# Kernel tuning notes

Hardware: AMD Instinct MI355X
Metric: run time of the kernel (lower is better)

Reference implementation:

```python
import jax, jax.numpy as jnp
import numpy as np

N = 50000
E = 800000
NDIM_IN = 128
NDIM_OUT = 64
H = 3
EDIM = 8
CLASS_NUM = 10
NEG_SLOPE = 0.2  # DGL GATConv default negative_slope


def _gat_layer(src, dst, x, W, a_l, a_r, b):
    """One DGL-style GATConv layer. x: [N, Fin]; W: [Fin, H*D]; a_l/a_r: [H, D]; b: [H*D]."""
    n, hd = x.shape[0], W.shape[1]
    D = hd // H
    f = (x @ W).reshape(n, H, D)                         # projected feats [N,H,D]
    el = (f * a_l[None]).sum(-1)                          # [N,H]
    er = (f * a_r[None]).sum(-1)                          # [N,H]
    e = jax.nn.leaky_relu(el[src] + er[dst], NEG_SLOPE)   # [E,H] per-edge logits
    m = jax.ops.segment_max(e, dst, num_segments=n)       # softmax max per dst node
    ex = jnp.exp(e - m[dst])                              # [E,H]
    denom = jax.ops.segment_sum(ex, dst, num_segments=n)  # [N,H]
    alpha = ex / denom[dst]                               # edge softmax
    out = jax.ops.segment_sum(f[src] * alpha[:, :, None], dst, num_segments=n)  # [N,H,D]
    return out + b.reshape(1, H, D)


def setup_inputs() -> dict:
    key = jax.random.key(0)
    ks = jax.random.split(key, 16)
    src = jax.random.randint(ks[0], (E,), 0, N)
    dst = jax.random.randint(ks[1], (E,), 0, N)
    nfeats = jax.random.normal(ks[2], (N, NDIM_IN), dtype=jnp.float32)
    efeats = jax.random.normal(ks[3], (E, EDIM), dtype=jnp.float32)
    s1 = 1.0 / np.sqrt(NDIM_IN)
    s2 = 1.0 / np.sqrt(H * NDIM_OUT)
    sp = 1.0 / np.sqrt(2 * H * NDIM_OUT)
    W1 = jax.random.normal(ks[4], (NDIM_IN, H * NDIM_OUT), dtype=jnp.float32) * s1
    al1 = jax.random.normal(ks[5], (H, NDIM_OUT), dtype=jnp.float32) * s1
    ar1 = jax.random.normal(ks[6], (H, NDIM_OUT), dtype=jnp.float32) * s1
    b1 = jnp.zeros((H * NDIM_OUT,), dtype=jnp.float32)
    W2 = jax.random.normal(ks[7], (H * NDIM_OUT, H * NDIM_OUT), dtype=jnp.float32) * s2
    al2 = jax.random.normal(ks[8], (H, NDIM_OUT), dtype=jnp.float32) * s2
    ar2 = jax.random.normal(ks[9], (H, NDIM_OUT), dtype=jnp.float32) * s2
    b2 = jnp.zeros((H * NDIM_OUT,), dtype=jnp.float32)
    Wp = jax.random.normal(ks[10], (2 * H * NDIM_OUT, CLASS_NUM), dtype=jnp.float32) * sp
    bp = jnp.zeros((CLASS_NUM,), dtype=jnp.float32)
    return {"src": src, "dst": dst, "nfeats": nfeats, "efeats": efeats,
            "W1": W1, "al1": al1, "ar1": ar1, "b1": b1,
            "W2": W2, "al2": al2, "ar2": ar2, "b2": b2,
            "Wp": Wp, "bp": bp}


def reference(src, dst, nfeats, efeats, W1, al1, ar1, b1, W2, al2, ar2, b2, Wp, bp):
    # efeats is accepted but unused, matching the original forward signature.
    h = _gat_layer(src, dst, nfeats, W1, al1, ar1, b1)      # [N,H,D]
    h = jax.nn.relu(h.reshape(h.shape[0], -1))              # [N,H*D]
    h = _gat_layer(src, dst, h, W2, al2, ar2, b2)           # [N,H,D]
    h = jax.nn.relu(h.reshape(h.shape[0], -1))              # [N,H*D]
    # MLPPredictor: per-edge concat(src,dst) -> linear
    score = jnp.concatenate([h[src], h[dst]], axis=1) @ Wp + bp  # [E,class_num]
    return score
```

## Files before the change

kernel.cpp:

```cpp
#include <hip/hip_runtime.h>
#include <cstdint>

constexpr int KIN = 128;
constexpr int HD  = 192;
constexpr int NC  = 10;
#define NEG_SLOPE 0.2f

typedef __attribute__((ext_vector_type(8))) short bf16x8;
typedef __attribute__((ext_vector_type(4))) float f32x4;

__device__ __forceinline__ float b2f(unsigned short u) {
    union { unsigned int i; float f; } x; x.i = ((unsigned int)u) << 16; return x.f;
}
__device__ __forceinline__ float b2f_lo(unsigned int u) {
    union { unsigned int i; float f; } x; x.i = u << 16; return x.f;
}
__device__ __forceinline__ float b2f_hi(unsigned int u) {
    union { unsigned int i; float f; } x; x.i = u & 0xffff0000u; return x.f;
}
__device__ __forceinline__ unsigned short f2b(float f) {
    union { float f; unsigned int i; } x; x.f = f;
    unsigned int r = x.i + 0x7FFFu + ((x.i >> 16) & 1u);
    return (unsigned short)(r >> 16);
}
__device__ __forceinline__ float gload(const void* p, long i, int isbf) {
    return isbf ? b2f(((const unsigned short*)p)[i]) : ((const float*)p)[i];
}
__device__ __forceinline__ float lrelu(float v) { return v > 0.f ? v : NEG_SLOPE * v; }

__global__ void k_prep(const void* __restrict__ nfeats, const void* __restrict__ W1,
                       const void* __restrict__ W2, const void* __restrict__ Wp,
                       unsigned short* __restrict__ xb, int* __restrict__ deg,
                       unsigned short* __restrict__ Bp1, unsigned short* __restrict__ Bp2,
                       unsigned short* __restrict__ BpPQ, int N, long nx,
                       int bZ, int bC, int* __restrict__ flag) {
    __shared__ int shIsb;
    if (threadIdx.x == 0) {
        const unsigned short* u = (const unsigned short*)W1;
        float mx = 0.f;
        for (int i = 0; i < 64; ++i) {
            float v = fabsf(b2f(u[i]));
            if (!(v < 1e30f)) v = 1e30f;
            mx = fmaxf(mx, v);
        }
        shIsb = (mx < 1e4f) ? 1 : 0;
        if (blockIdx.x == 0) *flag = shIsb;
    }
    __syncthreads();
    int isb = shIsb;
    int b = blockIdx.x, tid = threadIdx.x;
    if (b < bZ) { int i = b * 256 + tid; if (i < N) deg[i] = 0; return; }
    b -= bZ;
    if (b < bC) {
        if (isb) return;
        long i = (long)b * 256 + tid;
        if (i < nx) xb[i] = f2b(gload(nfeats, i, isb));
        return;
    }
    b -= bC;
    int t = b * 256 + tid;
    const int s1 = 12 * 4 * 512, s2 = s1 + 12 * 6 * 512, s3 = s2 + 6 * 512, s4 = s3 + 6 * 512;
    const void* W; unsigned short* Bp; int K, Creal, KS; long rowOff; int tt;
    if (t < s1)      { W = W1; Bp = Bp1;            K = KIN; Creal = HD; KS = 4; rowOff = 0;  tt = t; }
    else if (t < s2) { W = W2; Bp = Bp2;            K = HD;  Creal = HD; KS = 6; rowOff = 0;  tt = t - s1; }
    else if (t < s3) { W = Wp; Bp = BpPQ;           K = HD;  Creal = NC; KS = 6; rowOff = 0;  tt = t - s2; }
    else if (t < s4) { W = Wp; Bp = BpPQ + 6 * 512; K = HD;  Creal = NC; KS = 6; rowOff = HD; tt = t - s3; }
    else return;
    int j = tt & 7, lane = (tt >> 3) & 63, ks = (tt >> 9) % KS, ct = tt / (KS * 512);
    int k = ks * 32 + ((lane >> 4) << 3) + j;
    int c = ct * 16 + (lane & 15);
    float v = 0.f;
    if (k < K && c < Creal) v = gload(W, (rowOff + k) * (long)Creal + c, isb);
    Bp[tt] = f2b(v);
}

template<int CT, int KS, int ELR>
__global__ void k_mm(const void* __restrict__ Ain, const unsigned short* __restrict__ xbA,
                     const unsigned short* __restrict__ Bp,
                     unsigned short* __restrict__ fb, const void* __restrict__ al,
                     const void* __restrict__ ar, float* __restrict__ el4,
                     float* __restrict__ er4, int M, int Cout, const int* __restrict__ flag) {
    int wid = threadIdx.x >> 6, lane = threadIdx.x & 63;
    int rt = blockIdx.x * 4 + wid;
    if (rt * 16 >= M) return;
    int isb = *flag;
    const unsigned short* A = isb ? (const unsigned short*)Ain : xbA;
    const int K = KS * 32;
    int mrow = rt * 16 + (lane & 15);
    int kq = (lane >> 4) << 3;
    f32x4 acc[CT];
#pragma unroll
    for (int ct = 0; ct < CT; ++ct) acc[ct] = (f32x4){0.f, 0.f, 0.f, 0.f};
    const unsigned short* arow = A + (long)mrow * K + kq;
    const bf16x8* bp = (const bf16x8*)Bp;
#pragma unroll
    for (int ks = 0; ks < KS; ++ks) {
        bf16x8 a = *(const bf16x8*)(arow + ks * 32);
#pragma unroll
        for (int ct = 0; ct < CT; ++ct) {
            bf16x8 b = bp[(ct * KS + ks) * 64 + lane];
            acc[ct] = __builtin_amdgcn_mfma_f32_16x16x32_bf16(a, b, acc[ct], 0, 0, 0);
        }
    }
    int quad = lane >> 4, c0 = lane & 15;
    int rbase = rt * 16 + quad * 4;
#pragma unroll
    for (int ct = 0; ct < CT; ++ct)
#pragma unroll
        for (int r = 0; r < 4; ++r)
            fb[(long)(rbase + r) * Cout + ct * 16 + c0] = f2b(acc[ct][r]);
    if (ELR) {
        float pl[3][4], pr[3][4];
#pragma unroll
        for (int h = 0; h < 3; ++h)
#pragma unroll
            for (int r = 0; r < 4; ++r) { pl[h][r] = 0.f; pr[h][r] = 0.f; }
#pragma unroll
        for (int ct = 0; ct < CT; ++ct) {
            int h = ct >> 2;
            float wl = gload(al, ct * 16 + c0, isb);
            float wr = gload(ar, ct * 16 + c0, isb);
#pragma unroll
            for (int r = 0; r < 4; ++r) {
                pl[h][r] += acc[ct][r] * wl;
                pr[h][r] += acc[ct][r] * wr;
            }
        }
#pragma unroll
        for (int d = 1; d < 16; d <<= 1)
#pragma unroll
            for (int h = 0; h < 3; ++h)
#pragma unroll
                for (int r = 0; r < 4; ++r) {
                    pl[h][r] += __shfl_xor(pl[h][r], d);
                    pr[h][r] += __shfl_xor(pr[h][r], d);
                }
        if (c0 == 0) {
#pragma unroll
            for (int r = 0; r < 4; ++r)
#pragma unroll
                for (int h = 0; h < 3; ++h) {
                    el4[(long)(rbase + r) * 4 + h] = pl[h][r];
                    er4[(long)(rbase + r) * 4 + h] = pr[h][r];
                }
        }
    }
}

__global__ void k_mmpq(const unsigned short* __restrict__ A, const unsigned short* __restrict__ Bp,
                       unsigned short* __restrict__ Pb, unsigned short* __restrict__ Qb, int M) {
    constexpr int CT = 2, KS = 6;
    int wid = threadIdx.x >> 6, lane = threadIdx.x & 63;
    int rt = blockIdx.x * 4 + wid;
    if (rt * 16 >= M) return;
    const int K = KS * 32;
    int mrow = rt * 16 + (lane & 15);
    int kq = (lane >> 4) << 3;
    f32x4 acc[CT];
#pragma unroll
    for (int ct = 0; ct < CT; ++ct) acc[ct] = (f32x4){0.f, 0.f, 0.f, 0.f};
    const unsigned short* arow = A + (long)mrow * K + kq;
    const bf16x8* bp = (const bf16x8*)Bp;
#pragma unroll
    for (int ks = 0; ks < KS; ++ks) {
        bf16x8 a = *(const bf16x8*)(arow + ks * 32);
#pragma unroll
        for (int ct = 0; ct < CT; ++ct) {
            bf16x8 b = bp[(ct * KS + ks) * 64 + lane];
            acc[ct] = __builtin_amdgcn_mfma_f32_16x16x32_bf16(a, b, acc[ct], 0, 0, 0);
        }
    }
    int quad = lane >> 4, c0 = lane & 15;
    int rbase = rt * 16 + quad * 4;
    if (c0 < NC) {
#pragma unroll
        for (int r = 0; r < 4; ++r) {
            Pb[(long)(rbase + r) * 16 + c0] = f2b(acc[0][r]);
            Qb[(long)(rbase + r) * 16 + c0] = f2b(acc[1][r]);
        }
    }
}

__global__ void k_hist(const int* __restrict__ dst, int E, int* __restrict__ deg) {
    int i = blockIdx.x * blockDim.x + threadIdx.x;
    if (i < E) atomicAdd(&deg[dst[i]], 1);
}

__global__ void k_scan1(const int* __restrict__ deg, int n, int* __restrict__ off,
                        int* __restrict__ bsum) {
    __shared__ int sh[1024];
    int tid = threadIdx.x, i = blockIdx.x * 1024 + tid;
    int v = (i < n) ? deg[i] : 0;
    sh[tid] = v;
    __syncthreads();
    for (int s = 1; s < 1024; s <<= 1) {
        int t = (tid >= s) ? sh[tid - s] : 0;
        __syncthreads();
        sh[tid] += t;
        __syncthreads();
    }
    if (i < n) off[i] = sh[tid] - v;
    if (tid == 1023) bsum[blockIdx.x] = sh[tid];
}

__global__ void k_scan2(int* __restrict__ bsum, int nb, int* __restrict__ off, int n) {
    int tid = threadIdx.x;
    int v = (tid < nb) ? bsum[tid] : 0;
    int incl = v;
    for (int s = 1; s < 64; s <<= 1) {
        int t = __shfl_up(incl, s);
        if (tid >= s) incl += t;
    }
    if (tid < nb) bsum[tid] = incl - v;
    if (tid == 63) off[n] = incl;
}

__global__ void k_scan3(int* __restrict__ off, const int* __restrict__ bsum, int n,
                        int* __restrict__ cur) {
    int i = blockIdx.x * 1024 + threadIdx.x;
    if (i < n) {
        int v = off[i] + bsum[blockIdx.x];
        off[i] = v;
        cur[i] = v;
    }
}

__global__ void k_fill(const int* __restrict__ src, const int* __restrict__ dst, int E,
                       int* __restrict__ cur, int* __restrict__ csr) {
    int i = blockIdx.x * blockDim.x + threadIdx.x;
    if (i < E) {
        int p = atomicAdd(&cur[dst[i]], 1);
        csr[p] = src[i];
    }
}

__global__ void k_agg(const unsigned int* __restrict__ fbu, const float4* __restrict__ el4,
                      const float* __restrict__ er4, const int* __restrict__ off,
                      const int* __restrict__ csr, const void* __restrict__ bias,
                      unsigned int* __restrict__ outu, int Nn, const int* __restrict__ flag) {
    __shared__ float4 shW[4][64];
    int lane = threadIdx.x & 63;
    int wv = threadIdx.x >> 6;
    int n = blockIdx.x * 4 + wv;
    if (n >= Nn) return;
    int isb = *flag;
    int s0 = off[n], s1 = off[n + 1];
    int deg = s1 - s0;
    float er0 = er4[n * 4 + 0], er1 = er4[n * 4 + 1], er2 = er4[n * 4 + 2];
    int hsel = lane >> 4;
    float a0 = 0.f, a1 = 0.f, a2 = 0.f, a3 = 0.f;

    if (deg <= 64) {
        bool on = lane < deg;
        int sIdx = on ? csr[s0 + lane] : 0;
        float4 el = el4[sIdx];
        float t0 = on ? lrelu(el.x + er0) : -1e30f;
        float t1 = on ? lrelu(el.y + er1) : -1e30f;
        float t2 = on ? lrelu(el.z + er2) : -1e30f;
        float m0 = t0, m1 = t1, m2 = t2;
        for (int d = 1; d < 64; d <<= 1) {
            m0 = fmaxf(m0, __shfl_xor(m0, d));
            m1 = fmaxf(m1, __shfl_xor(m1, d));
            m2 = fmaxf(m2, __shfl_xor(m2, d));
        }
        float w0 = on ? __expf(t0 - m0) : 0.f;
        float w1 = on ? __expf(t1 - m1) : 0.f;
        float w2 = on ? __expf(t2 - m2) : 0.f;
        float d0 = w0, d1 = w1, d2 = w2;
        for (int d = 1; d < 64; d <<= 1) {
            d0 += __shfl_xor(d0, d);
            d1 += __shfl_xor(d1, d);
            d2 += __shfl_xor(d2, d);
        }
        w0 *= 1.f / d0; w1 *= 1.f / d1; w2 *= 1.f / d2;
        shW[wv][lane] = make_float4(__int_as_float(sIdx), w0, w1, w2);
        if (lane < 48) {
            const float4* wr = shW[wv];
            long lb = 2 * lane;
            int j = 0;
            for (; j + 4 <= deg; j += 4) {
                float4 r0 = wr[j], r1 = wr[j + 1], r2 = wr[j + 2], r3 = wr[j + 3];
                uint2 u0 = *(const uint2*)(fbu + (long)__float_as_int(r0.x) * 96 + lb);
                uint2 u1 = *(const uint2*)(fbu + (long)__float_as_int(r1.x) * 96 + lb);
                uint2 u2 = *(const uint2*)(fbu + (long)__float_as_int(r2.x) * 96 + lb);
                uint2 u3 = *(const uint2*)(fbu + (long)__float_as_int(r3.x) * 96 + lb);
                float q0 = hsel == 0 ? r0.y : (hsel == 1 ? r0.z : r0.w);
                float q1 = hsel == 0 ? r1.y : (hsel == 1 ? r1.z : r1.w);
                float q2 = hsel == 0 ? r2.y : (hsel == 1 ? r2.z : r2.w);
                float q3 = hsel == 0 ? r3.y : (hsel == 1 ? r3.z : r3.w);
                a0 += q0 * b2f_lo(u0.x); a1 += q0 * b2f_hi(u0.x);
                a2 += q0 * b2f_lo(u0.y); a3 += q0 * b2f_hi(u0.y);
                a0 += q1 * b2f_lo(u1.x); a1 += q1 * b2f_hi(u1.x);
                a2 += q1 * b2f_lo(u1.y); a3 += q1 * b2f_hi(u1.y);
                a0 += q2 * b2f_lo(u2.x); a1 += q2 * b2f_hi(u2.x);
                a2 += q2 * b2f_lo(u2.y); a3 += q2 * b2f_hi(u2.y);
                a0 += q3 * b2f_lo(u3.x); a1 += q3 * b2f_hi(u3.x);
                a2 += q3 * b2f_lo(u3.y); a3 += q3 * b2f_hi(u3.y);
            }
            for (; j < deg; ++j) {
                float4 r0 = wr[j];
                uint2 u0 = *(const uint2*)(fbu + (long)__float_as_int(r0.x) * 96 + lb);
                float q0 = hsel == 0 ? r0.y : (hsel == 1 ? r0.z : r0.w);
                a0 += q0 * b2f_lo(u0.x); a1 += q0 * b2f_hi(u0.x);
                a2 += q0 * b2f_lo(u0.y); a3 += q0 * b2f_hi(u0.y);
            }
        }
    } else {
        float m0 = -1e30f, m1 = -1e30f, m2 = -1e30f;
        for (int e = s0 + lane; e < s1; e += 64) {
            float4 el = el4[csr[e]];
            m0 = fmaxf(m0, lrelu(el.x + er0));
            m1 = fmaxf(m1, lrelu(el.y + er1));
            m2 = fmaxf(m2, lrelu(el.z + er2));
        }
        for (int d = 1; d < 64; d <<= 1) {
            m0 = fmaxf(m0, __shfl_xor(m0, d));
            m1 = fmaxf(m1, __shfl_xor(m1, d));
            m2 = fmaxf(m2, __shfl_xor(m2, d));
        }
        float d0 = 0.f, d1 = 0.f, d2 = 0.f;
        for (int e = s0 + lane; e < s1; e += 64) {
            float4 el = el4[csr[e]];
            d0 += __expf(lrelu(el.x + er0) - m0);
            d1 += __expf(lrelu(el.y + er1) - m1);
            d2 += __expf(lrelu(el.z + er2) - m2);
        }
        for (int d = 1; d < 64; d <<= 1) {
            d0 += __shfl_xor(d0, d);
            d1 += __shfl_xor(d1, d);
            d2 += __shfl_xor(d2, d);
        }
        if (lane < 48) {
            float mh  = hsel == 0 ? m0 : (hsel == 1 ? m1 : m2);
            float dh  = hsel == 0 ? d0 : (hsel == 1 ? d1 : d2);
            float erh = hsel == 0 ? er0 : (hsel == 1 ? er1 : er2);
            float idh = 1.f / dh;
            long lb = 2 * lane;
            for (int e = s0; e < s1; ++e) {
                int s = csr[e];
                float4 el = el4[s];
                float eh = hsel == 0 ? el.x : (hsel == 1 ? el.y : el.z);
                float w = __expf(lrelu(eh + erh) - mh) * idh;
                uint2 u = *(const uint2*)(fbu + (long)s * 96 + lb);
                a0 += w * b2f_lo(u.x); a1 += w * b2f_hi(u.x);
                a2 += w * b2f_lo(u.y); a3 += w * b2f_hi(u.y);
            }
        }
    }
    if (lane < 48) {
        int c = 4 * lane;
        a0 = fmaxf(a0 + gload(bias, c,     isb), 0.f);
        a1 = fmaxf(a1 + gload(bias, c + 1, isb), 0.f);
        a2 = fmaxf(a2 + gload(bias, c + 2, isb), 0.f);
        a3 = fmaxf(a3 + gload(bias, c + 3, isb), 0.f);
        uint2 o;
        o.x = (unsigned)f2b(a0) | ((unsigned)f2b(a1) << 16);
        o.y = (unsigned)f2b(a2) | ((unsigned)f2b(a3) << 16);
        *(uint2*)(outu + (long)n * 96 + 2 * lane) = o;
    }
}

__global__ void k_score(const int* __restrict__ src, const int* __restrict__ dst,
                        const unsigned int* __restrict__ Pu, const unsigned int* __restrict__ Qu,
                        const void* __restrict__ bp, void* __restrict__ out,
                        int E, const int* __restrict__ flag) {
    __shared__ float sh[512 * NC];
    int tid = threadIdx.x;
    int e0 = blockIdx.x * 512;
    int isb = *flag;
    float bb[NC];
#pragma unroll
    for (int c = 0; c < NC; ++c) bb[c] = gload(bp, c, isb);

    float v[2][NC];
#pragma unroll
    for (int k = 0; k < 2; ++k) {
        int e = e0 + tid + k * 256;
        if (e < E) {
            const uint4* p4 = (const uint4*)(Pu + (long)src[e] * 8);
            const uint4* q4 = (const uint4*)(Qu + (long)dst[e] * 8);
            uint4 pa = p4[0]; unsigned int pb_ = Pu[(long)src[e] * 8 + 4];
            uint4 qa = q4[0]; unsigned int qb_ = Qu[(long)dst[e] * 8 + 4];
            v[k][0] = b2f_lo(pa.x) + b2f_lo(qa.x) + bb[0];
            v[k][1] = b2f_hi(pa.x) + b2f_hi(qa.x) + bb[1];
            v[k][2] = b2f_lo(pa.y) + b2f_lo(qa.y) + bb[2];
            v[k][3] = b2f_hi(pa.y) + b2f_hi(qa.y) + bb[3];
            v[k][4] = b2f_lo(pa.z) + b2f_lo(qa.z) + bb[4];
            v[k][5] = b2f_hi(pa.z) + b2f_hi(qa.z) + bb[5];
            v[k][6] = b2f_lo(pa.w) + b2f_lo(qa.w) + bb[6];
            v[k][7] = b2f_hi(pa.w) + b2f_hi(qa.w) + bb[7];
            v[k][8] = b2f_lo(pb_)  + b2f_lo(qb_)  + bb[8];
            v[k][9] = b2f_hi(pb_)  + b2f_hi(qb_)  + bb[9];
        }
    }
    int nE = min(512, E - e0);
    if (isb) {
        unsigned int* shu = (unsigned int*)sh;
#pragma unroll
        for (int k = 0; k < 2; ++k) {
            int le = tid + k * 256;
            if (e0 + le < E) {
#pragma unroll
                for (int c = 0; c < NC / 2; ++c)
                    shu[le * (NC / 2) + c] =
                        (unsigned)f2b(v[k][2 * c]) | ((unsigned)f2b(v[k][2 * c + 1]) << 16);
            }
        }
        __syncthreads();
        int nU = nE * (NC / 2);
        unsigned int* ob = (unsigned int*)((unsigned short*)out + (long)e0 * NC);
        int nU4 = nU >> 2;
        uint4* ob4 = (uint4*)ob;
        const uint4* sb4 = (const uint4*)shu;
        for (int u = tid; u < nU4; u += 256) ob4[u] = sb4[u];
        for (int w = (nU4 << 2) + tid; w < nU; w += 256) ob[w] = shu[w];
    } else {
#pragma unroll
        for (int k = 0; k < 2; ++k) {
            int le = tid + k * 256;
            if (e0 + le < E) {
#pragma unroll
                for (int c = 0; c < NC; ++c) sh[le * NC + c] = v[k][c];
            }
        }
        __syncthreads();
        int nU = nE * NC;
        float* ob = (float*)out + (long)e0 * NC;
        int nU4 = nU >> 2;
        float4* ob4 = (float4*)ob;
        const float4* sb4 = (const float4*)sh;
        for (int u = tid; u < nU4; u += 256) ob4[u] = sb4[u];
        for (int w = (nU4 << 2) + tid; w < nU; w += 256) ob[w] = sh[w];
    }
}

extern "C" void kernel_launch(void* const* d_in, const int* in_sizes, int n_in,
                              void* d_out, int out_size, void* d_ws, size_t ws_size,
                              hipStream_t stream) {
    const int* src = (const int*)d_in[0];
    const int* dst = (const int*)d_in[1];
    const void* nfeats = d_in[2];
    const void* W1  = d_in[4];
    const void* al1 = d_in[5];
    const void* ar1 = d_in[6];
    const void* b1  = d_in[7];
    const void* W2  = d_in[8];
    const void* al2 = d_in[9];
    const void* ar2 = d_in[10];
    const void* b2  = d_in[11];
    const void* Wp  = d_in[12];
    const void* bp  = d_in[13];

    const int E = in_sizes[0];
    const int N = in_sizes[2] / KIN;

    size_t o = 0;
    auto alloc = [&](size_t bytes) { size_t r = o; o = (o + bytes + 255) & ~(size_t)255; return r; };
    char* ws = (char*)d_ws;
    int*   flag = (int*)  (ws + alloc(4));
    int*   deg  = (int*)  (ws + alloc((size_t)N * 4));
    int*   off  = (int*)  (ws + alloc((size_t)(N + 1) * 4));
    int*   cur  = (int*)  (ws + alloc((size_t)N * 4));
    int*   bsum = (int*)  (ws + alloc(64 * 4));
    int*   csr  = (int*)  (ws + alloc((size_t)E * 4));
    unsigned short* xb  = (unsigned short*)(ws + alloc((size_t)N * KIN * 2));
    unsigned short* fb  = (unsigned short*)(ws + alloc((size_t)N * HD * 2));
    unsigned short* hb  = (unsigned short*)(ws + alloc((size_t)N * HD * 2));
    unsigned short* Bp1 = (unsigned short*)(ws + alloc((size_t)12 * 4 * 512 * 2));
    unsigned short* Bp2 = (unsigned short*)(ws + alloc((size_t)12 * 6 * 512 * 2));
    unsigned short* BpPQ= (unsigned short*)(ws + alloc((size_t)2 * 6 * 512 * 2));
    float* el4  = (float*)(ws + alloc((size_t)N * 16));
    float* er4  = (float*)(ws + alloc((size_t)N * 16));
    unsigned short* Pb = (unsigned short*)(ws + alloc((size_t)N * 16 * 2));
    unsigned short* Qb = (unsigned short*)(ws + alloc((size_t)N * 16 * 2));
    (void)ws_size; (void)n_in; (void)out_size;

    const int TB = 256;
    long nx = (long)N * KIN;
    int gE   = (E + TB - 1) / TB;
    int gSc  = (E + 511) / 512;
    int gAgg = (N + 3) / 4;
    int rowTiles = (N + 15) / 16;
    int gMM  = (rowTiles + 3) / 4;
    int nb   = (N + 1023) / 1024;

    int bZ = (N + TB - 1) / TB;
    int bC = (int)((nx + TB - 1) / TB);
    int bP = (12 * 4 * 512 + 12 * 6 * 512 + 2 * 6 * 512 + TB - 1) / TB;
    k_prep<<<bZ + bC + bP, TB, 0, stream>>>(nfeats, W1, W2, Wp, xb, deg,
                                            Bp1, Bp2, BpPQ, N, nx, bZ, bC, flag);

    k_hist<<<gE, TB, 0, stream>>>(dst, E, deg);
    k_scan1<<<nb, 1024, 0, stream>>>(deg, N, off, bsum);
    k_scan2<<<1, 64, 0, stream>>>(bsum, nb, off, N);
    k_scan3<<<nb, 1024, 0, stream>>>(off, bsum, N, cur);
    k_fill<<<gE, TB, 0, stream>>>(src, dst, E, cur, csr);

    k_mm<12, 4, 1><<<gMM, TB, 0, stream>>>(nfeats, xb, Bp1, fb, al1, ar1, el4, er4, N, HD, flag);
    k_agg<<<gAgg, TB, 0, stream>>>((const unsigned int*)fb, (const float4*)el4, er4,
                                   off, csr, b1, (unsigned int*)hb, N, flag);

    k_mm<12, 6, 1><<<gMM, TB, 0, stream>>>(hb, hb, Bp2, fb, al2, ar2, el4, er4, N, HD, flag);
    k_agg<<<gAgg, TB, 0, stream>>>((const unsigned int*)fb, (const float4*)el4, er4,
                                   off, csr, b2, (unsigned int*)hb, N, flag);

    k_mmpq<<<gMM, TB, 0, stream>>>(hb, BpPQ, Pb, Qb, N);
    k_score<<<gSc, TB, 0, stream>>>(src, dst, (const unsigned int*)Pb, (const unsigned int*)Qb,
                                    bp, d_out, E, flag);
}
```

Measured before the change: 398.4 us.

## Split degree counters into 8 partitions per node to reduce atomic contention

Each destination node now has 8 degree and cursor counters, chosen by block index, so the histogram and CSR fill atomics spread over 8x more addresses. The scan runs over the expanded N*8 array, which keeps each node's partitions contiguous, and the aggregation reads node offsets at stride 8. Each thread now handles 4 edges. The cost is a larger scan (400k entries), a 1024-thread second-level scan, more zeroing work, and a bigger workspace.

```diff
diff --git a/kernel.cpp b/kernel.cpp
--- a/kernel.cpp
+++ b/kernel.cpp
@@ -30,9 +30,9 @@
 
 __global__ void k_prep(const void* __restrict__ nfeats, const void* __restrict__ W1,
                        const void* __restrict__ W2, const void* __restrict__ Wp,
-                       unsigned short* __restrict__ xb, int* __restrict__ deg,
+                       unsigned short* __restrict__ xb, int* __restrict__ deg8,
                        unsigned short* __restrict__ Bp1, unsigned short* __restrict__ Bp2,
-                       unsigned short* __restrict__ BpPQ, int N, long nx,
+                       unsigned short* __restrict__ BpPQ, int n8, long nx,
                        int bZ, int bC, int* __restrict__ flag) {
     __shared__ int shIsb;
     if (threadIdx.x == 0) {
@@ -49,7 +49,7 @@
     __syncthreads();
     int isb = shIsb;
     int b = blockIdx.x, tid = threadIdx.x;
-    if (b < bZ) { int i = b * 256 + tid; if (i < N) deg[i] = 0; return; }
+    if (b < bZ) { int i = b * 256 + tid; if (i < n8) deg8[i] = 0; return; }
     b -= bZ;
     if (b < bC) {
         if (isb) return;
@@ -181,16 +181,21 @@
     }
 }
 
-__global__ void k_hist(const int* __restrict__ dst, int E, int* __restrict__ deg) {
-    int i = blockIdx.x * blockDim.x + threadIdx.x;
-    if (i < E) atomicAdd(&deg[dst[i]], 1);
-}
-
-__global__ void k_scan1(const int* __restrict__ deg, int n, int* __restrict__ off,
+__global__ void k_hist(const int* __restrict__ dst, int E, int* __restrict__ deg8) {
+    int part = blockIdx.x & 7;
+    int base = blockIdx.x * 1024 + threadIdx.x;
+#pragma unroll
+    for (int k = 0; k < 4; ++k) {
+        int i = base + k * 256;
+        if (i < E) atomicAdd(&deg8[dst[i] * 8 + part], 1);
+    }
+}
+
+__global__ void k_scan1(const int* __restrict__ deg8, int n, int* __restrict__ off,
                         int* __restrict__ bsum) {
     __shared__ int sh[1024];
     int tid = threadIdx.x, i = blockIdx.x * 1024 + tid;
-    int v = (i < n) ? deg[i] : 0;
+    int v = (i < n) ? deg8[i] : 0;
     sh[tid] = v;
     __syncthreads();
     for (int s = 1; s < 1024; s <<= 1) {
@@ -204,15 +209,19 @@
 }
 
 __global__ void k_scan2(int* __restrict__ bsum, int nb, int* __restrict__ off, int n) {
+    __shared__ int sh[1024];
     int tid = threadIdx.x;
     int v = (tid < nb) ? bsum[tid] : 0;
-    int incl = v;
-    for (int s = 1; s < 64; s <<= 1) {
-        int t = __shfl_up(incl, s);
-        if (tid >= s) incl += t;
-    }
-    if (tid < nb) bsum[tid] = incl - v;
-    if (tid == 63) off[n] = incl;
+    sh[tid] = v;
+    __syncthreads();
+    for (int s = 1; s < 1024; s <<= 1) {
+        int t = (tid >= s) ? sh[tid - s] : 0;
+        __syncthreads();
+        sh[tid] += t;
+        __syncthreads();
+    }
+    if (tid < nb) bsum[tid] = sh[tid] - v;
+    if (tid == 1023) off[n] = sh[1023];
 }
 
 __global__ void k_scan3(int* __restrict__ off, const int* __restrict__ bsum, int n,
@@ -226,16 +235,21 @@
 }
 
 __global__ void k_fill(const int* __restrict__ src, const int* __restrict__ dst, int E,
-                       int* __restrict__ cur, int* __restrict__ csr) {
-    int i = blockIdx.x * blockDim.x + threadIdx.x;
-    if (i < E) {
-        int p = atomicAdd(&cur[dst[i]], 1);
-        csr[p] = src[i];
+                       int* __restrict__ cur8, int* __restrict__ csr) {
+    int part = blockIdx.x & 7;
+    int base = blockIdx.x * 1024 + threadIdx.x;
+#pragma unroll
+    for (int k = 0; k < 4; ++k) {
+        int i = base + k * 256;
+        if (i < E) {
+            int p = atomicAdd(&cur8[dst[i] * 8 + part], 1);
+            csr[p] = src[i];
+        }
     }
 }
 
 __global__ void k_agg(const unsigned int* __restrict__ fbu, const float4* __restrict__ el4,
-                      const float* __restrict__ er4, const int* __restrict__ off,
+                      const float* __restrict__ er4, const int* __restrict__ off8,
                       const int* __restrict__ csr, const void* __restrict__ bias,
                       unsigned int* __restrict__ outu, int Nn, const int* __restrict__ flag) {
     __shared__ float4 shW[4][64];
@@ -244,7 +258,7 @@
     int n = blockIdx.x * 4 + wv;
     if (n >= Nn) return;
     int isb = *flag;
-    int s0 = off[n], s1 = off[n + 1];
+    int s0 = off8[n * 8], s1 = off8[n * 8 + 8];
     int deg = s1 - s0;
     float er0 = er4[n * 4 + 0], er1 = er4[n * 4 + 1], er2 = er4[n * 4 + 2];
     int hsel = lane >> 4;
@@ -453,15 +467,16 @@
 
     const int E = in_sizes[0];
     const int N = in_sizes[2] / KIN;
+    const int n8 = N * 8;
 
     size_t o = 0;
     auto alloc = [&](size_t bytes) { size_t r = o; o = (o + bytes + 255) & ~(size_t)255; return r; };
     char* ws = (char*)d_ws;
     int*   flag = (int*)  (ws + alloc(4));
-    int*   deg  = (int*)  (ws + alloc((size_t)N * 4));
-    int*   off  = (int*)  (ws + alloc((size_t)(N + 1) * 4));
-    int*   cur  = (int*)  (ws + alloc((size_t)N * 4));
-    int*   bsum = (int*)  (ws + alloc(64 * 4));
+    int*   deg8 = (int*)  (ws + alloc((size_t)n8 * 4));
+    int*   off8 = (int*)  (ws + alloc((size_t)(n8 + 1) * 4));
+    int*   cur8 = (int*)  (ws + alloc((size_t)n8 * 4));
+    int*   bsum = (int*)  (ws + alloc(1024 * 4));
     int*   csr  = (int*)  (ws + alloc((size_t)E * 4));
     unsigned short* xb  = (unsigned short*)(ws + alloc((size_t)N * KIN * 2));
     unsigned short* fb  = (unsigned short*)(ws + alloc((size_t)N * HD * 2));
@@ -477,32 +492,32 @@
 
     const int TB = 256;
     long nx = (long)N * KIN;
-    int gE   = (E + TB - 1) / TB;
+    int gE4  = (E + 1023) / 1024;
     int gSc  = (E + 511) / 512;
     int gAgg = (N + 3) / 4;
     int rowTiles = (N + 15) / 16;
     int gMM  = (rowTiles + 3) / 4;
-    int nb   = (N + 1023) / 1024;
-
-    int bZ = (N + TB - 1) / TB;
+    int nb   = (n8 + 1023) / 1024;
+
+    int bZ = (n8 + TB - 1) / TB;
     int bC = (int)((nx + TB - 1) / TB);
     int bP = (12 * 4 * 512 + 12 * 6 * 512 + 2 * 6 * 512 + TB - 1) / TB;
-    k_prep<<<bZ + bC + bP, TB, 0, stream>>>(nfeats, W1, W2, Wp, xb, deg,
-                                            Bp1, Bp2, BpPQ, N, nx, bZ, bC, flag);
-
-    k_hist<<<gE, TB, 0, stream>>>(dst, E, deg);
-    k_scan1<<<nb, 1024, 0, stream>>>(deg, N, off, bsum);
-    k_scan2<<<1, 64, 0, stream>>>(bsum, nb, off, N);
-    k_scan3<<<nb, 1024, 0, stream>>>(off, bsum, N, cur);
-    k_fill<<<gE, TB, 0, stream>>>(src, dst, E, cur, csr);
+    k_prep<<<bZ + bC + bP, TB, 0, stream>>>(nfeats, W1, W2, Wp, xb, deg8,
+                                            Bp1, Bp2, BpPQ, n8, nx, bZ, bC, flag);
+
+    k_hist<<<gE4, TB, 0, stream>>>(dst, E, deg8);
+    k_scan1<<<nb, 1024, 0, stream>>>(deg8, n8, off8, bsum);
+    k_scan2<<<1, 1024, 0, stream>>>(bsum, nb, off8, n8);
+    k_scan3<<<nb, 1024, 0, stream>>>(off8, bsum, n8, cur8);
+    k_fill<<<gE4, TB, 0, stream>>>(src, dst, E, cur8, csr);
 
     k_mm<12, 4, 1><<<gMM, TB, 0, stream>>>(nfeats, xb, Bp1, fb, al1, ar1, el4, er4, N, HD, flag);
     k_agg<<<gAgg, TB, 0, stream>>>((const unsigned int*)fb, (const float4*)el4, er4,
-                                   off, csr, b1, (unsigned int*)hb, N, flag);
+                                   off8, csr, b1, (unsigned int*)hb, N, flag);
 
     k_mm<12, 6, 1><<<gMM, TB, 0, stream>>>(hb, hb, Bp2, fb, al2, ar2, el4, er4, N, HD, flag);
     k_agg<<<gAgg, TB, 0, stream>>>((const unsigned int*)fb, (const float4*)el4, er4,
-                                   off, csr, b2, (unsigned int*)hb, N, flag);
+                                   off8, csr, b2, (unsigned int*)hb, N, flag);
 
     k_mmpq<<<gMM, TB, 0, stream>>>(hb, BpPQ, Pb, Qb, N);
     k_score<<<gSc, TB, 0, stream>>>(src, dst, (const unsigned int*)Pb, (const unsigned int*)Qb,
```

Result: slower. 417.1 us (+4.7%).
